# Performance work log

Hardware: AMD Instinct MI355X
Metric: run time of the kernel (lower is better)

Reference implementation:

```python
import math
import jax, jax.numpy as jnp
import numpy as np

B, S, T, C, H = 4, 100, 128, 256, 256
NH, DH = 4, 32            # num_attention_heads//2, hidden_size//num_attention_heads
AH = NH * DH              # all_head_size = 128
FH = 32                   # fire_hidden_size
MAX_SP, MAX_TM, MAX_DOY = 180.0, 365.0, 182.0


def _fire(dist, c, w1, w2, max_dist):
    # FIREDistanceBias: log-compressed distance -> MLP(1->FH, SiLU, FH->1, no bias)
    c = jnp.maximum(c, 0.0)
    d = jnp.log(c * dist + 1.0) / jnp.log(c * max_dist + 1.0)
    h = jax.nn.silu(d[..., None] * w1[:, 0])   # (..., FH)
    return h @ w2[0]                            # (...,)


def setup_inputs() -> dict:
    key = jax.random.key(0)
    ks = jax.random.split(key, 20)
    p = 0.02
    inp = {
        "hidden_states": jax.random.normal(ks[0], (B, S, T, H), jnp.float32),
        "source_embeddings": jax.random.normal(ks[1], (B, S, C, H), jnp.float32),
        "attention_mask": jnp.zeros((B, 1, 1, T, C), jnp.float32),
        "st_dist": jax.random.uniform(ks[2], (B, T, C, 2), jnp.float32)
                   * jnp.array([MAX_SP, MAX_TM], jnp.float32),
        "st_doy_dist": jax.random.uniform(ks[3], (B, T, C), jnp.float32) * MAX_DOY,
        # attention projections (Linear H->AH with bias), output dense (AH->H)
        "Wq": jax.random.normal(ks[4], (AH, H), jnp.float32) * p,
        "bq": jnp.zeros((AH,), jnp.float32),
        "Wk": jax.random.normal(ks[5], (AH, H), jnp.float32) * p,
        "bk": jnp.zeros((AH,), jnp.float32),
        "Wv": jax.random.normal(ks[6], (AH, H), jnp.float32) * p,
        "bv": jnp.zeros((AH,), jnp.float32),
        "Wo": jax.random.normal(ks[7], (H, AH), jnp.float32) * p,
        "bo": jnp.zeros((H,), jnp.float32),
        # FIRE params: spatial / temporal / seasonal
        "c_s": jnp.float32(100.0),
        "w1_s": jax.random.normal(ks[8], (FH, 1), jnp.float32) * 0.5,
        "w2_s": jax.random.normal(ks[9], (1, FH), jnp.float32) * 0.5,
        "c_t": jnp.float32(100.0),
        "w1_t": jax.random.normal(ks[10], (FH, 1), jnp.float32) * 0.5,
        "w2_t": jax.random.normal(ks[11], (1, FH), jnp.float32) * 0.5,
        "c_d": jnp.float32(100.0),
        "w1_d": jax.random.normal(ks[12], (FH, 1), jnp.float32) * 0.5,
        "w2_d": jax.random.normal(ks[13], (1, FH), jnp.float32) * 0.5,
        # per-species log scales (init zeros in torch)
        "s_log_scale": jnp.zeros((S,), jnp.float32),
        "t_log_scale": jnp.zeros((S,), jnp.float32),
    }
    return inp


def reference(hidden_states, source_embeddings, attention_mask, st_dist, st_doy_dist,
              Wq, bq, Wk, bk, Wv, bv, Wo, bo,
              c_s, w1_s, w2_s, c_t, w1_t, w2_t, c_d, w1_d, w2_d,
              s_log_scale, t_log_scale):
    # FIRE distance biases over (B, T, C)
    sb = _fire(st_dist[..., 0], c_s, w1_s, w2_s, MAX_SP)
    tb = _fire(st_dist[..., 1], c_t, w1_t, w2_t, MAX_TM)
    db = _fire(st_doy_dist, c_d, w1_d, w2_d, MAX_DOY)
    # (B, S, T, C): species-scaled spatial+temporal + seasonal bias
    bias = (sb[:, None] * jnp.exp(s_log_scale)[None, :, None, None]
            + tb[:, None] * jnp.exp(t_log_scale)[None, :, None, None]
            + db[:, None])

    # projections; split heads: (B,S,L,AH) -> (B,S,NH,L,DH)
    q = (hidden_states @ Wq.T + bq).reshape(B, S, T, NH, DH).transpose(0, 1, 3, 2, 4)
    k = (source_embeddings @ Wk.T + bk).reshape(B, S, C, NH, DH).transpose(0, 1, 3, 2, 4)
    v = (source_embeddings @ Wv.T + bv).reshape(B, S, C, NH, DH).transpose(0, 1, 3, 2, 4)

    scores = jnp.einsum('bshtd,bshcd->bshtc', q, k) / math.sqrt(DH)
    scores = scores + attention_mask + bias[:, :, None]   # mask (B,1,1,T,C), bias (B,S,1,T,C)
    probs = jax.nn.softmax(scores, axis=-1)
    ctx = jnp.einsum('bshtc,bshcd->bshtd', probs, v)
    ctx = ctx.transpose(0, 1, 3, 2, 4).reshape(B, S, T, AH)
    return ctx @ Wo.T + bo   # STCrossOutput dense (dropout=0, eval)
```

## Files before the change

### kernel.cpp

```cpp
#include <hip/hip_runtime.h>
#include <hip/hip_bf16.h>
#include <math.h>

#define Bdim 4
#define Sdim 100
#define Tdim 128
#define Cdim 256
#define Hdim 256
#define NHd  4
#define DHd  32
#define AHd  128

typedef short bf16x8 __attribute__((ext_vector_type(8)));
typedef float f32x4 __attribute__((ext_vector_type(4)));

#define WAITCNT_V(n) do { \
  asm volatile("s_waitcnt vmcnt(" #n ")" ::: "memory"); \
  __builtin_amdgcn_sched_barrier(0); \
} while (0)

__device__ __forceinline__ short f2b(float x) {
  unsigned u = __float_as_uint(x);
  unsigned r = (u + 0x7FFF + ((u >> 16) & 1)) >> 16;
  return (short)r;
}

__device__ __forceinline__ void split2(float x, short& hi, short& lo) {
  unsigned u = __float_as_uint(x) & 0xFFFF0000u;
  hi = (short)(u >> 16);
  lo = f2b(x - __uint_as_float(u));
}

__device__ __forceinline__ float fire_eval(float dist, float c,
                                           const float* __restrict__ w1,
                                           const float* __restrict__ w2,
                                           float maxd) {
  c = fmaxf(c, 0.0f);
  float d = logf(fmaf(c, dist, 1.0f)) / logf(fmaf(c, maxd, 1.0f));
  float acc = 0.0f;
#pragma unroll
  for (int j = 0; j < 32; ++j) {
    float x = d * w1[j];
    float h = x / (1.0f + expf(-x));
    acc = fmaf(h, w2[j], acc);
  }
  return acc;
}

__global__ __launch_bounds__(256) void fire_bias_kernel(
    const float* __restrict__ st_dist, const float* __restrict__ st_doy,
    const float* __restrict__ mask,
    const float* __restrict__ c_s, const float* __restrict__ w1_s, const float* __restrict__ w2_s,
    const float* __restrict__ c_t, const float* __restrict__ w1_t, const float* __restrict__ w2_t,
    const float* __restrict__ c_d, const float* __restrict__ w1_d, const float* __restrict__ w2_d,
    float4* __restrict__ pk) {
  int i = blockIdx.x * 256 + threadIdx.x;
  if (i >= Bdim * Tdim * Cdim) return;
  float2 dv = ((const float2*)st_dist)[i];
  float4 r;
  r.x = fire_eval(dv.x, c_s[0], w1_s, w2_s, 180.0f);
  r.y = fire_eval(dv.y, c_t[0], w1_t, w2_t, 365.0f);
  r.z = fire_eval(st_doy[i], c_d[0], w1_d, w2_d, 182.0f) + mask[i];
  r.w = 0.0f;
  pk[i] = r;
}

__global__ __launch_bounds__(256) void bias_combine(
    const float4* __restrict__ pk,
    const float* __restrict__ sls, const float* __restrict__ tls,
    float* __restrict__ bF) {
  const int l = threadIdx.x & 63;
  const int lr = l & 15, lg = l >> 4;
  const int nt = blockIdx.x * 4 + (threadIdx.x >> 6);
  const int wt = blockIdx.y;
  const int b  = blockIdx.z;
  const int c = nt * 16 + lr;
  float sb[4], tb[4], db[4];
#pragma unroll
  for (int r = 0; r < 4; ++r) {
    float4 v = pk[(size_t)b * Tdim * Cdim + (size_t)(wt * 16 + lg * 4 + r) * Cdim + c];
    sb[r] = v.x; tb[r] = v.y; db[r] = v.z;
  }
  for (int s = 0; s < Sdim; ++s) {
    float es = __expf(sls[s]), et = __expf(tls[s]);
    float4 o;
    o.x = fmaf(sb[0], es, fmaf(tb[0], et, db[0]));
    o.y = fmaf(sb[1], es, fmaf(tb[1], et, db[1]));
    o.z = fmaf(sb[2], es, fmaf(tb[2], et, db[2]));
    o.w = fmaf(sb[3], es, fmaf(tb[3], et, db[3]));
    size_t idx = ((((size_t)(b * Sdim + s) * 8 + wt) * 16 + nt) * 64 + l);
    *(float4*)(bF + idx * 4) = o;
  }
}

__global__ __launch_bounds__(256) void wsplit_pack(
    const float* __restrict__ Wq, const float* __restrict__ Wk,
    const float* __restrict__ Wv, const float* __restrict__ Wo,
    short* __restrict__ pack) {
  int which = blockIdx.y;
  const float* W = which == 0 ? Wq : which == 1 ? Wk : which == 2 ? Wv : Wo;
  int idx = blockIdx.x * 256 + threadIdx.x;
  int j = idx & 7;
  int l = (idx >> 3) & 63;
  int frag = idx >> 9;
  int nt, kk8, Kd;
  if (which == 3) { nt = frag & 15; kk8 = frag >> 4; Kd = 128; }
  else           { nt = frag & 7;  kk8 = frag >> 3; Kd = 256; }
  int n = nt * 16 + (l & 15);
  int k = kk8 * 32 + (l >> 4) * 8 + j;
  float val = W[(size_t)n * Kd + k];
  short h, lo_;
  if (which == 3) split2(val, h, lo_);
  else { h = f2b(val); lo_ = 0; }
  pack[(size_t)which * 65536 + idx] = h;
  pack[(size_t)which * 65536 + 32768 + idx] = lo_;
}


__global__ __launch_bounds__(256, 2) void proj_q_mfma(
    const float* __restrict__ A, const short* __restrict__ Wp,
    const float* __restrict__ bias, short* __restrict__ O, float scale) {
  __shared__ short wlds[2][8 * 512];
  const int tid = threadIdx.x;
  const int l = tid & 63, w = tid >> 6;
  const int lr = l & 15, lg = l >> 4;
  const int m0 = blockIdx.x * 128;
  const float* ap0 = A + (size_t)(m0 + w * 32 + lr) * 256 + lg * 8;
  const float* ap1 = ap0 + (size_t)16 * 256;

  auto stage = [&](int buf, int kk) {
#pragma unroll
    for (int r = 0; r < 2; ++r) {
      int f = w + 4 * r;
      const short* gsrc = Wp + ((size_t)(kk * 8 + f) * 64 + l) * 8;
      int loff = __builtin_amdgcn_readfirstlane(buf * 4096 + f * 512);
      __builtin_amdgcn_global_load_lds(gsrc, &wlds[0][0] + loff, 16, 0, 0);
    }
  };

  f32x4 acc[2][8] = {};
  stage(0, 0);
  float4 c0a = *(const float4*)ap0;
  float4 c0b = *(const float4*)(ap0 + 4);
  float4 c1a = *(const float4*)ap1;
  float4 c1b = *(const float4*)(ap1 + 4);
#pragma unroll
  for (int kk = 0; kk < 8; ++kk) {
    const int buf = kk & 1;
    float4 n0a, n0b, n1a, n1b;
    if (kk < 7) {
      stage(buf ^ 1, kk + 1);
      const int nk = (kk + 1) * 32;
      n0a = *(const float4*)(ap0 + nk);
      n0b = *(const float4*)(ap0 + nk + 4);
      n1a = *(const float4*)(ap1 + nk);
      n1b = *(const float4*)(ap1 + nk + 4);
    }
    bf16x8 af[2];
    {
      float a0[8] = {c0a.x, c0a.y, c0a.z, c0a.w, c0b.x, c0b.y, c0b.z, c0b.w};
      float a1[8] = {c1a.x, c1a.y, c1a.z, c1a.w, c1b.x, c1b.y, c1b.z, c1b.w};
#pragma unroll
      for (int e = 0; e < 8; ++e) { af[0][e] = f2b(a0[e]); af[1][e] = f2b(a1[e]); }
    }
    if (kk < 7) { WAITCNT_V(6); } else { WAITCNT_V(0); }
    __builtin_amdgcn_s_barrier();
    const short* lb = &wlds[0][0] + buf * 4096 + l * 8;
#pragma unroll
    for (int nt = 0; nt < 8; ++nt) {
      bf16x8 wv = *(const bf16x8*)(lb + nt * 512);
#pragma unroll
      for (int mi = 0; mi < 2; ++mi)
        acc[mi][nt] = __builtin_amdgcn_mfma_f32_16x16x32_bf16(af[mi], wv, acc[mi][nt], 0, 0, 0);
    }
    __builtin_amdgcn_s_barrier();
    if (kk < 7) { c0a = n0a; c0b = n0b; c1a = n1a; c1b = n1b; }
  }
#pragma unroll
  for (int mi = 0; mi < 2; ++mi)
#pragma unroll
    for (int nt = 0; nt < 8; ++nt)
#pragma unroll
      for (int r = 0; r < 4; ++r)
        O[(size_t)(m0 + w * 32 + mi * 16 + lg * 4 + r) * 128 + nt * 16 + lr] =
            f2b((acc[mi][nt][r] + bias[nt * 16 + lr]) * scale);
}

__global__ __launch_bounds__(256, 2) void proj_kv_mfma(
    const float* __restrict__ A,
    const short* __restrict__ Wkp, const float* __restrict__ bk,
    const short* __restrict__ Wvp, const float* __restrict__ bv,
    short* __restrict__ Ko, short* __restrict__ Vo) {
  __shared__ short wlds[2][16 * 512];
  const int tid = threadIdx.x;
  const int l = tid & 63, w = tid >> 6;
  const int lr = l & 15, lg = l >> 4;
  const int m0 = blockIdx.x * 128;
  const float* ap0 = A + (size_t)(m0 + w * 32 + lr) * 256 + lg * 8;
  const float* ap1 = ap0 + (size_t)16 * 256;

  auto stage = [&](int buf, int kk) {
#pragma unroll
    for (int r = 0; r < 4; ++r) {
      int f = w + 4 * r;
      const short* gsrc = ((f >> 3) ? Wvp : Wkp) + ((size_t)(kk * 8 + (f & 7)) * 64 + l) * 8;
      int loff = __builtin_amdgcn_readfirstlane(buf * 8192 + f * 512);
      __builtin_amdgcn_global_load_lds(gsrc, &wlds[0][0] + loff, 16, 0, 0);
    }
  };

  f32x4 accK[2][8] = {}, accV[2][8] = {};
  stage(0, 0);
  float4 c0a = *(const float4*)ap0;
  float4 c0b = *(const float4*)(ap0 + 4);
  float4 c1a = *(const float4*)ap1;
  float4 c1b = *(const float4*)(ap1 + 4);
#pragma unroll
  for (int kk = 0; kk < 8; ++kk) {
    const int buf = kk & 1;
    float4 n0a, n0b, n1a, n1b;
    if (kk < 7) {
      stage(buf ^ 1, kk + 1);
      const int nk = (kk + 1) * 32;
      n0a = *(const float4*)(ap0 + nk);
      n0b = *(const float4*)(ap0 + nk + 4);
      n1a = *(const float4*)(ap1 + nk);
      n1b = *(const float4*)(ap1 + nk + 4);
    }
    bf16x8 af[2];
    {
      float a0[8] = {c0a.x, c0a.y, c0a.z, c0a.w, c0b.x, c0b.y, c0b.z, c0b.w};
      float a1[8] = {c1a.x, c1a.y, c1a.z, c1a.w, c1b.x, c1b.y, c1b.z, c1b.w};
#pragma unroll
      for (int e = 0; e < 8; ++e) { af[0][e] = f2b(a0[e]); af[1][e] = f2b(a1[e]); }
    }
    if (kk < 7) { WAITCNT_V(8); } else { WAITCNT_V(0); }
    __builtin_amdgcn_s_barrier();
    const short* lb = &wlds[0][0] + buf * 8192 + l * 8;
#pragma unroll
    for (int nt = 0; nt < 8; ++nt) {
      bf16x8 kw = *(const bf16x8*)(lb + nt * 512);
      bf16x8 vw = *(const bf16x8*)(lb + (8 + nt) * 512);
#pragma unroll
      for (int mi = 0; mi < 2; ++mi) {
        accK[mi][nt] = __builtin_amdgcn_mfma_f32_16x16x32_bf16(af[mi], kw, accK[mi][nt], 0, 0, 0);
        accV[mi][nt] = __builtin_amdgcn_mfma_f32_16x16x32_bf16(af[mi], vw, accV[mi][nt], 0, 0, 0);
      }
    }
    __builtin_amdgcn_s_barrier();
    if (kk < 7) { c0a = n0a; c0b = n0b; c1a = n1a; c1b = n1b; }
  }
#pragma unroll
  for (int mi = 0; mi < 2; ++mi)
#pragma unroll
    for (int nt = 0; nt < 8; ++nt)
#pragma unroll
      for (int r = 0; r < 4; ++r) {
        size_t row = (size_t)(m0 + w * 32 + mi * 16 + lg * 4 + r) * 128 + nt * 16 + lr;
        Ko[row] = f2b(accK[mi][nt][r] + bk[nt * 16 + lr]);
        Vo[row] = f2b(accV[mi][nt][r] + bv[nt * 16 + lr]);
      }
}

__global__ __launch_bounds__(256, 2) void proj_o_mfma(
    const short* __restrict__ Ahi, const short* __restrict__ Alo,
    const short* __restrict__ Wp, const float* __restrict__ bias,
    float* __restrict__ O) {
  __shared__ short wlds[2][32 * 512];
  const int tid = threadIdx.x;
  const int l = tid & 63, w = tid >> 6;
  const int lr = l & 15, lg = l >> 4;
  const int m0 = blockIdx.x * 128;
  const short* ah0 = Ahi + (size_t)(m0 + w * 32 + lr) * 128 + lg * 8;
  const short* al0 = Alo + (size_t)(m0 + w * 32 + lr) * 128 + lg * 8;
  const short* ah1 = ah0 + (size_t)16 * 128;
  const short* al1 = al0 + (size_t)16 * 128;

  auto stage = [&](int buf, int kk) {
#pragma unroll
    for (int r = 0; r < 8; ++r) {
      int f = w + 4 * r;
      const short* gsrc = Wp + ((f >> 4) ? 32768 : 0)
                          + ((size_t)(kk * 16 + (f & 15)) * 64 + l) * 8;
      int loff = __builtin_amdgcn_readfirstlane(buf * 16384 + f * 512);
      __builtin_amdgcn_global_load_lds(gsrc, &wlds[0][0] + loff, 16, 0, 0);
    }
  };

  f32x4 acc[2][16] = {};
  stage(0, 0);
  bf16x8 ch0 = *(const bf16x8*)ah0;
  bf16x8 cl0 = *(const bf16x8*)al0;
  bf16x8 ch1 = *(const bf16x8*)ah1;
  bf16x8 cl1 = *(const bf16x8*)al1;
#pragma unroll
  for (int kk = 0; kk < 4; ++kk) {
    const int buf = kk & 1;
    bf16x8 nh0, nl0, nh1, nl1;
    if (kk < 3) {
      stage(buf ^ 1, kk + 1);
      const int nk = (kk + 1) * 32;
      nh0 = *(const bf16x8*)(ah0 + nk);
      nl0 = *(const bf16x8*)(al0 + nk);
      nh1 = *(const bf16x8*)(ah1 + nk);
      nl1 = *(const bf16x8*)(al1 + nk);
    }
    if (kk < 3) { WAITCNT_V(12); } else { WAITCNT_V(0); }
    __builtin_amdgcn_s_barrier();
    bf16x8 ahi[2] = {ch0, ch1};
    bf16x8 alo[2] = {cl0, cl1};
    const short* lb = &wlds[0][0] + buf * 16384 + l * 8;
#pragma unroll
    for (int nt = 0; nt < 16; ++nt) {
      bf16x8 whi = *(const bf16x8*)(lb + nt * 512);
      bf16x8 wlo = *(const bf16x8*)(lb + (16 + nt) * 512);
#pragma unroll
      for (int mi = 0; mi < 2; ++mi) {
        acc[mi][nt] = __builtin_amdgcn_mfma_f32_16x16x32_bf16(ahi[mi], whi, acc[mi][nt], 0, 0, 0);
        acc[mi][nt] = __builtin_amdgcn_mfma_f32_16x16x32_bf16(ahi[mi], wlo, acc[mi][nt], 0, 0, 0);
        acc[mi][nt] = __builtin_amdgcn_mfma_f32_16x16x32_bf16(alo[mi], whi, acc[mi][nt], 0, 0, 0);
      }
    }
    __builtin_amdgcn_s_barrier();
    if (kk < 3) { ch0 = nh0; cl0 = nl0; ch1 = nh1; cl1 = nl1; }
  }
#pragma unroll
  for (int mi = 0; mi < 2; ++mi)
#pragma unroll
    for (int nt = 0; nt < 16; ++nt)
#pragma unroll
      for (int r = 0; r < 4; ++r)
        O[(size_t)(m0 + w * 32 + mi * 16 + lg * 4 + r) * 256 + nt * 16 + lr] =
            acc[mi][nt][r] + bias[nt * 16 + lr];
}

__global__ __launch_bounds__(512, 2) void attn_mfma(
    const short* __restrict__ Qb, const short* __restrict__ Kb,
    const short* __restrict__ Vb,
    const float* __restrict__ bF,
    short* __restrict__ Chi, short* __restrict__ Clo) {
  __shared__ short vfrag[8][2][64][8];
  __shared__ short pbuf[8][16 * 36];

  const int tid = threadIdx.x;
  const int l = tid & 63;
  const int w = tid >> 6;
  const int lr = l & 15, lg = l >> 4;
  const int bid = blockIdx.x;
  const int xcd = bid & 7;
  const int i_  = bid >> 3;
  const int bs  = xcd * 50 + (i_ >> 2);
  const int h   = i_ & 3;

  const size_t kvbase = (size_t)bs * Cdim * AHd + h * DHd;
  const size_t qbase  = (size_t)bs * Tdim * AHd + h * DHd;

#pragma unroll
  for (int rep = 0; rep < 2; ++rep) {
    int chunk = tid * 2 + rep;
    int c = chunk >> 2, q = chunk & 3;
    bf16x8 v8 = *(const bf16x8*)(Vb + kvbase + (size_t)c * AHd + q * 8);
    int kc = c >> 5, nt = q >> 1;
    int lanebase = ((c & 31) >> 3) * 16 + (q & 1) * 8;
    int j = c & 7;
#pragma unroll
    for (int e = 0; e < 8; ++e) {
      int row = lanebase + e;
      int prow = row ^ ((row >> 4) << 1);
      vfrag[kc][nt][prow][j] = v8[e];
    }
  }
  __syncthreads();

  bf16x8 qf = *(const bf16x8*)(Qb + qbase + (size_t)(w * 16 + lr) * AHd + lg * 8);
  bf16x8 kf[16];
#pragma unroll
  for (int nt = 0; nt < 16; ++nt)
    kf[nt] = *(const bf16x8*)(Kb + kvbase + (size_t)(nt * 16 + lr) * AHd + lg * 8);

  const float4* bb = (const float4*)bF + ((size_t)bs * 8 + w) * 16 * 64 + l;
  f32x4 sacc[16];
#pragma unroll
  for (int nt = 0; nt < 16; ++nt) {
    float4 cv = bb[nt * 64];
    f32x4 cinit = {cv.x, cv.y, cv.z, cv.w};
    sacc[nt] = __builtin_amdgcn_mfma_f32_16x16x32_bf16(qf, kf[nt], cinit, 0, 0, 0);
  }

  float rinv[4];
#pragma unroll
  for (int nt = 0; nt < 16; ++nt)
#pragma unroll
    for (int r = 0; r < 4; ++r)
      sacc[nt][r] = __expf(sacc[nt][r]);
#pragma unroll
  for (int r = 0; r < 4; ++r) {
    float su = 0.f;
#pragma unroll
    for (int nt = 0; nt < 16; ++nt) su += sacc[nt][r];
#pragma unroll
    for (int off = 1; off < 16; off <<= 1) su += __shfl_xor(su, off);
    rinv[r] = 1.0f / su;
  }

  const f32x4 zero = {0.f, 0.f, 0.f, 0.f};
  f32x4 cacc[2] = {zero, zero};
  short* pb = &pbuf[w][0];
  const int lp = l ^ ((l >> 4) << 1);
#pragma unroll
  for (int kc = 0; kc < 8; ++kc) {
#pragma unroll
    for (int ntl = 0; ntl < 2; ++ntl) {
      int nt = kc * 2 + ntl;
#pragma unroll
      for (int r = 0; r < 4; ++r)
        pb[(lg * 4 + r) * 36 + ntl * 16 + lr] = f2b(sacc[nt][r]);
    }
    bf16x8 af = *(const bf16x8*)&pb[lr * 36 + lg * 8];
#pragma unroll
    for (int ntd = 0; ntd < 2; ++ntd) {
      bf16x8 vf = *(const bf16x8*)&vfrag[kc][ntd][lp][0];
      cacc[ntd] = __builtin_amdgcn_mfma_f32_16x16x32_bf16(af, vf, cacc[ntd], 0, 0, 0);
    }
  }

#pragma unroll
  for (int ntd = 0; ntd < 2; ++ntd)
#pragma unroll
    for (int r = 0; r < 4; ++r) {
      float val = cacc[ntd][r] * rinv[r];
      short h_, lo_;
      split2(val, h_, lo_);
      size_t idx = qbase + (size_t)(w * 16 + lg * 4 + r) * AHd + ntd * 16 + lr;
      Chi[idx] = h_;
      Clo[idx] = lo_;
    }
}

extern "C" void kernel_launch(void* const* d_in, const int* in_sizes, int n_in,
                              void* d_out, int out_size, void* d_ws, size_t ws_size,
                              hipStream_t stream) {
  const float* hs     = (const float*)d_in[0];
  const float* se     = (const float*)d_in[1];
  const float* mask   = (const float*)d_in[2];
  const float* stdist = (const float*)d_in[3];
  const float* stdoy  = (const float*)d_in[4];
  const float* Wq = (const float*)d_in[5];
  const float* bq = (const float*)d_in[6];
  const float* Wk = (const float*)d_in[7];
  const float* bk = (const float*)d_in[8];
  const float* Wv = (const float*)d_in[9];
  const float* bv = (const float*)d_in[10];
  const float* Wo = (const float*)d_in[11];
  const float* bo = (const float*)d_in[12];
  const float* c_s  = (const float*)d_in[13];
  const float* w1_s = (const float*)d_in[14];
  const float* w2_s = (const float*)d_in[15];
  const float* c_t  = (const float*)d_in[16];
  const float* w1_t = (const float*)d_in[17];
  const float* w2_t = (const float*)d_in[18];
  const float* c_d  = (const float*)d_in[19];
  const float* w1_d = (const float*)d_in[20];
  const float* w2_d = (const float*)d_in[21];
  const float* sls  = (const float*)d_in[22];
  const float* tls  = (const float*)d_in[23];
  float* out = (float*)d_out;

  float* ws = (float*)d_ws;
  const size_t BTC  = (size_t)Bdim * Tdim * Cdim;
  const size_t BSTC = (size_t)Bdim * Sdim * Tdim * Cdim;
  const size_t NQ   = (size_t)Bdim * Sdim * Tdim * AHd;
  const size_t NKV  = (size_t)Bdim * Sdim * Cdim * AHd;

  float4* pk  = (float4*)ws;
  float* bF   = ws + 4 * BTC;
  short* wpck = (short*)(bF + BSTC);
  short* Qb   = wpck + 262144;
  short* Kb   = Qb + NQ;
  short* Vb   = Kb + NKV;
  short* Chi  = Vb + NKV;
  short* Clo  = Chi + NQ;

  const int MQ  = Bdim * Sdim * Tdim;
  const int MKV = Bdim * Sdim * Cdim;

  fire_bias_kernel<<<(Bdim * Tdim * Cdim + 255) / 256, 256, 0, stream>>>(
      stdist, stdoy, mask, c_s, w1_s, w2_s, c_t, w1_t, w2_t, c_d, w1_d, w2_d, pk);

  bias_combine<<<dim3(4, 8, Bdim), 256, 0, stream>>>(pk, sls, tls, bF);

  wsplit_pack<<<dim3(128, 4), 256, 0, stream>>>(Wq, Wk, Wv, Wo, wpck);

  proj_q_mfma<<<dim3(MQ / 128), 256, 0, stream>>>(hs, wpck, bq, Qb,
                                                  0.17677669529663687f);
  proj_kv_mfma<<<dim3(MKV / 128), 256, 0, stream>>>(
      se, wpck + 65536, bk, wpck + 131072, bv, Kb, Vb);

  attn_mfma<<<dim3(Bdim * Sdim * NHd), 512, 0, stream>>>(
      Qb, Kb, Vb, bF, Chi, Clo);

  proj_o_mfma<<<dim3(MQ / 128), 256, 0, stream>>>(Chi, Clo, wpck + 196608, bo, out);
}
```

Measured before the change: 158.7 us.

## Merge Q, KV projections and bias combine into one launch; hoist Q/K loads

Combines the separate bias_combine, proj_q_mfma and proj_kv_mfma kernels into one kernel, phase1, whose blocks branch on block index to do KV projection, Q projection or bias expansion. This removes two launches and the tail gaps between them, so the short bias work can run alongside the GEMM blocks. In the attention kernel, the Q and K fragment global loads are moved ahead of the V staging into LDS so their latency overlaps it. In exchange the Q path now reserves the larger KV-sized LDS buffer, which may lower occupancy for those blocks, and the mixed block types can leave the load unevenly spread across CUs.

```diff
diff --git a/kernel.cpp b/kernel.cpp
--- a/kernel.cpp
+++ b/kernel.cpp
@@ -63,34 +63,6 @@
   r.z = fire_eval(st_doy[i], c_d[0], w1_d, w2_d, 182.0f) + mask[i];
   r.w = 0.0f;
   pk[i] = r;
-}
-
-__global__ __launch_bounds__(256) void bias_combine(
-    const float4* __restrict__ pk,
-    const float* __restrict__ sls, const float* __restrict__ tls,
-    float* __restrict__ bF) {
-  const int l = threadIdx.x & 63;
-  const int lr = l & 15, lg = l >> 4;
-  const int nt = blockIdx.x * 4 + (threadIdx.x >> 6);
-  const int wt = blockIdx.y;
-  const int b  = blockIdx.z;
-  const int c = nt * 16 + lr;
-  float sb[4], tb[4], db[4];
-#pragma unroll
-  for (int r = 0; r < 4; ++r) {
-    float4 v = pk[(size_t)b * Tdim * Cdim + (size_t)(wt * 16 + lg * 4 + r) * Cdim + c];
-    sb[r] = v.x; tb[r] = v.y; db[r] = v.z;
-  }
-  for (int s = 0; s < Sdim; ++s) {
-    float es = __expf(sls[s]), et = __expf(tls[s]);
-    float4 o;
-    o.x = fmaf(sb[0], es, fmaf(tb[0], et, db[0]));
-    o.y = fmaf(sb[1], es, fmaf(tb[1], et, db[1]));
-    o.z = fmaf(sb[2], es, fmaf(tb[2], et, db[2]));
-    o.w = fmaf(sb[3], es, fmaf(tb[3], et, db[3]));
-    size_t idx = ((((size_t)(b * Sdim + s) * 8 + wt) * 16 + nt) * 64 + l);
-    *(float4*)(bF + idx * 4) = o;
-  }
 }
 
 __global__ __launch_bounds__(256) void wsplit_pack(
@@ -116,150 +88,172 @@
   pack[(size_t)which * 65536 + 32768 + idx] = lo_;
 }
 
-
-__global__ __launch_bounds__(256, 2) void proj_q_mfma(
-    const float* __restrict__ A, const short* __restrict__ Wp,
-    const float* __restrict__ bias, short* __restrict__ O, float scale) {
-  __shared__ short wlds[2][8 * 512];
+__global__ __launch_bounds__(256, 2) void phase1(
+    const float* __restrict__ se,
+    const short* __restrict__ Wkp, const float* __restrict__ bk,
+    const short* __restrict__ Wvp, const float* __restrict__ bv,
+    short* __restrict__ Ko, short* __restrict__ Vo,
+    const float* __restrict__ hs, const short* __restrict__ Wqp,
+    const float* __restrict__ bq, short* __restrict__ Qb, float scale,
+    const float4* __restrict__ pk,
+    const float* __restrict__ sls, const float* __restrict__ tls,
+    float* __restrict__ bF) {
+  __shared__ short wlds[2][16 * 512];
+  const int bid = blockIdx.x;
   const int tid = threadIdx.x;
   const int l = tid & 63, w = tid >> 6;
   const int lr = l & 15, lg = l >> 4;
-  const int m0 = blockIdx.x * 128;
-  const float* ap0 = A + (size_t)(m0 + w * 32 + lr) * 256 + lg * 8;
-  const float* ap1 = ap0 + (size_t)16 * 256;
-
-  auto stage = [&](int buf, int kk) {
-#pragma unroll
-    for (int r = 0; r < 2; ++r) {
-      int f = w + 4 * r;
-      const short* gsrc = Wp + ((size_t)(kk * 8 + f) * 64 + l) * 8;
-      int loff = __builtin_amdgcn_readfirstlane(buf * 4096 + f * 512);
-      __builtin_amdgcn_global_load_lds(gsrc, &wlds[0][0] + loff, 16, 0, 0);
-    }
-  };
-
-  f32x4 acc[2][8] = {};
-  stage(0, 0);
-  float4 c0a = *(const float4*)ap0;
-  float4 c0b = *(const float4*)(ap0 + 4);
-  float4 c1a = *(const float4*)ap1;
-  float4 c1b = *(const float4*)(ap1 + 4);
-#pragma unroll
-  for (int kk = 0; kk < 8; ++kk) {
-    const int buf = kk & 1;
-    float4 n0a, n0b, n1a, n1b;
-    if (kk < 7) {
-      stage(buf ^ 1, kk + 1);
-      const int nk = (kk + 1) * 32;
-      n0a = *(const float4*)(ap0 + nk);
-      n0b = *(const float4*)(ap0 + nk + 4);
-      n1a = *(const float4*)(ap1 + nk);
-      n1b = *(const float4*)(ap1 + nk + 4);
-    }
-    bf16x8 af[2];
-    {
-      float a0[8] = {c0a.x, c0a.y, c0a.z, c0a.w, c0b.x, c0b.y, c0b.z, c0b.w};
-      float a1[8] = {c1a.x, c1a.y, c1a.z, c1a.w, c1b.x, c1b.y, c1b.z, c1b.w};
-#pragma unroll
-      for (int e = 0; e < 8; ++e) { af[0][e] = f2b(a0[e]); af[1][e] = f2b(a1[e]); }
-    }
-    if (kk < 7) { WAITCNT_V(6); } else { WAITCNT_V(0); }
-    __builtin_amdgcn_s_barrier();
-    const short* lb = &wlds[0][0] + buf * 4096 + l * 8;
-#pragma unroll
-    for (int nt = 0; nt < 8; ++nt) {
-      bf16x8 wv = *(const bf16x8*)(lb + nt * 512);
-#pragma unroll
-      for (int mi = 0; mi < 2; ++mi)
-        acc[mi][nt] = __builtin_amdgcn_mfma_f32_16x16x32_bf16(af[mi], wv, acc[mi][nt], 0, 0, 0);
-    }
-    __builtin_amdgcn_s_barrier();
-    if (kk < 7) { c0a = n0a; c0b = n0b; c1a = n1a; c1b = n1b; }
-  }
-#pragma unroll
-  for (int mi = 0; mi < 2; ++mi)
-#pragma unroll
-    for (int nt = 0; nt < 8; ++nt)
-#pragma unroll
-      for (int r = 0; r < 4; ++r)
-        O[(size_t)(m0 + w * 32 + mi * 16 + lg * 4 + r) * 128 + nt * 16 + lr] =
-            f2b((acc[mi][nt][r] + bias[nt * 16 + lr]) * scale);
-}
-
-__global__ __launch_bounds__(256, 2) void proj_kv_mfma(
-    const float* __restrict__ A,
-    const short* __restrict__ Wkp, const float* __restrict__ bk,
-    const short* __restrict__ Wvp, const float* __restrict__ bv,
-    short* __restrict__ Ko, short* __restrict__ Vo) {
-  __shared__ short wlds[2][16 * 512];
-  const int tid = threadIdx.x;
-  const int l = tid & 63, w = tid >> 6;
-  const int lr = l & 15, lg = l >> 4;
-  const int m0 = blockIdx.x * 128;
-  const float* ap0 = A + (size_t)(m0 + w * 32 + lr) * 256 + lg * 8;
-  const float* ap1 = ap0 + (size_t)16 * 256;
-
-  auto stage = [&](int buf, int kk) {
+
+  if (bid < 800) {
+    const int m0 = bid * 128;
+    const float* ap0 = se + (size_t)(m0 + w * 32 + lr) * 256 + lg * 8;
+    const float* ap1 = ap0 + (size_t)16 * 256;
+
+    auto stage = [&](int buf, int kk) {
+#pragma unroll
+      for (int r = 0; r < 4; ++r) {
+        int f = w + 4 * r;
+        const short* gsrc = ((f >> 3) ? Wvp : Wkp) + ((size_t)(kk * 8 + (f & 7)) * 64 + l) * 8;
+        int loff = __builtin_amdgcn_readfirstlane(buf * 8192 + f * 512);
+        __builtin_amdgcn_global_load_lds(gsrc, &wlds[0][0] + loff, 16, 0, 0);
+      }
+    };
+
+    f32x4 accK[2][8] = {}, accV[2][8] = {};
+    stage(0, 0);
+    float4 c0a = *(const float4*)ap0;
+    float4 c0b = *(const float4*)(ap0 + 4);
+    float4 c1a = *(const float4*)ap1;
+    float4 c1b = *(const float4*)(ap1 + 4);
+#pragma unroll
+    for (int kk = 0; kk < 8; ++kk) {
+      const int buf = kk & 1;
+      float4 n0a, n0b, n1a, n1b;
+      if (kk < 7) {
+        stage(buf ^ 1, kk + 1);
+        const int nk = (kk + 1) * 32;
+        n0a = *(const float4*)(ap0 + nk);
+        n0b = *(const float4*)(ap0 + nk + 4);
+        n1a = *(const float4*)(ap1 + nk);
+        n1b = *(const float4*)(ap1 + nk + 4);
+      }
+      bf16x8 af[2];
+      {
+        float a0[8] = {c0a.x, c0a.y, c0a.z, c0a.w, c0b.x, c0b.y, c0b.z, c0b.w};
+        float a1[8] = {c1a.x, c1a.y, c1a.z, c1a.w, c1b.x, c1b.y, c1b.z, c1b.w};
+#pragma unroll
+        for (int e = 0; e < 8; ++e) { af[0][e] = f2b(a0[e]); af[1][e] = f2b(a1[e]); }
+      }
+      if (kk < 7) { WAITCNT_V(8); } else { WAITCNT_V(0); }
+      __builtin_amdgcn_s_barrier();
+      const short* lb = &wlds[0][0] + buf * 8192 + l * 8;
+#pragma unroll
+      for (int nt = 0; nt < 8; ++nt) {
+        bf16x8 kw = *(const bf16x8*)(lb + nt * 512);
+        bf16x8 vw = *(const bf16x8*)(lb + (8 + nt) * 512);
+#pragma unroll
+        for (int mi = 0; mi < 2; ++mi) {
+          accK[mi][nt] = __builtin_amdgcn_mfma_f32_16x16x32_bf16(af[mi], kw, accK[mi][nt], 0, 0, 0);
+          accV[mi][nt] = __builtin_amdgcn_mfma_f32_16x16x32_bf16(af[mi], vw, accV[mi][nt], 0, 0, 0);
+        }
+      }
+      __builtin_amdgcn_s_barrier();
+      if (kk < 7) { c0a = n0a; c0b = n0b; c1a = n1a; c1b = n1b; }
+    }
+#pragma unroll
+    for (int mi = 0; mi < 2; ++mi)
+#pragma unroll
+      for (int nt = 0; nt < 8; ++nt)
+#pragma unroll
+        for (int r = 0; r < 4; ++r) {
+          size_t row = (size_t)(m0 + w * 32 + mi * 16 + lg * 4 + r) * 128 + nt * 16 + lr;
+          Ko[row] = f2b(accK[mi][nt][r] + bk[nt * 16 + lr]);
+          Vo[row] = f2b(accV[mi][nt][r] + bv[nt * 16 + lr]);
+        }
+  } else if (bid < 1200) {
+    const int m0 = (bid - 800) * 128;
+    const float* ap0 = hs + (size_t)(m0 + w * 32 + lr) * 256 + lg * 8;
+    const float* ap1 = ap0 + (size_t)16 * 256;
+
+    auto stage = [&](int buf, int kk) {
+#pragma unroll
+      for (int r = 0; r < 2; ++r) {
+        int f = w + 4 * r;
+        const short* gsrc = Wqp + ((size_t)(kk * 8 + f) * 64 + l) * 8;
+        int loff = __builtin_amdgcn_readfirstlane(buf * 8192 + f * 512);
+        __builtin_amdgcn_global_load_lds(gsrc, &wlds[0][0] + loff, 16, 0, 0);
+      }
+    };
+
+    f32x4 acc[2][8] = {};
+    stage(0, 0);
+    float4 c0a = *(const float4*)ap0;
+    float4 c0b = *(const float4*)(ap0 + 4);
+    float4 c1a = *(const float4*)ap1;
+    float4 c1b = *(const float4*)(ap1 + 4);
+#pragma unroll
+    for (int kk = 0; kk < 8; ++kk) {
+      const int buf = kk & 1;
+      float4 n0a, n0b, n1a, n1b;
+      if (kk < 7) {
+        stage(buf ^ 1, kk + 1);
+        const int nk = (kk + 1) * 32;
+        n0a = *(const float4*)(ap0 + nk);
+        n0b = *(const float4*)(ap0 + nk + 4);
+        n1a = *(const float4*)(ap1 + nk);
+        n1b = *(const float4*)(ap1 + nk + 4);
+      }
+      bf16x8 af[2];
+      {
+        float a0[8] = {c0a.x, c0a.y, c0a.z, c0a.w, c0b.x, c0b.y, c0b.z, c0b.w};
+        float a1[8] = {c1a.x, c1a.y, c1a.z, c1a.w, c1b.x, c1b.y, c1b.z, c1b.w};
+#pragma unroll
+        for (int e = 0; e < 8; ++e) { af[0][e] = f2b(a0[e]); af[1][e] = f2b(a1[e]); }
+      }
+      if (kk < 7) { WAITCNT_V(6); } else { WAITCNT_V(0); }
+      __builtin_amdgcn_s_barrier();
+      const short* lb = &wlds[0][0] + buf * 8192 + l * 8;
+#pragma unroll
+      for (int nt = 0; nt < 8; ++nt) {
+        bf16x8 wv = *(const bf16x8*)(lb + nt * 512);
+#pragma unroll
+        for (int mi = 0; mi < 2; ++mi)
+          acc[mi][nt] = __builtin_amdgcn_mfma_f32_16x16x32_bf16(af[mi], wv, acc[mi][nt], 0, 0, 0);
+      }
+      __builtin_amdgcn_s_barrier();
+      if (kk < 7) { c0a = n0a; c0b = n0b; c1a = n1a; c1b = n1b; }
+    }
+#pragma unroll
+    for (int mi = 0; mi < 2; ++mi)
+#pragma unroll
+      for (int nt = 0; nt < 8; ++nt)
+#pragma unroll
+        for (int r = 0; r < 4; ++r)
+          Qb[(size_t)(m0 + w * 32 + mi * 16 + lg * 4 + r) * 128 + nt * 16 + lr] =
+              f2b((acc[mi][nt][r] + bq[nt * 16 + lr]) * scale);
+  } else {
+    const int bb_ = bid - 1200;
+    const int nt = (bb_ & 3) * 4 + w;
+    const int wt = (bb_ >> 2) & 7;
+    const int b  = bb_ >> 5;
+    const int c = nt * 16 + lr;
+    float sb[4], tb[4], db[4];
 #pragma unroll
     for (int r = 0; r < 4; ++r) {
-      int f = w + 4 * r;
-      const short* gsrc = ((f >> 3) ? Wvp : Wkp) + ((size_t)(kk * 8 + (f & 7)) * 64 + l) * 8;
-      int loff = __builtin_amdgcn_readfirstlane(buf * 8192 + f * 512);
-      __builtin_amdgcn_global_load_lds(gsrc, &wlds[0][0] + loff, 16, 0, 0);
-    }
-  };
-
-  f32x4 accK[2][8] = {}, accV[2][8] = {};
-  stage(0, 0);
-  float4 c0a = *(const float4*)ap0;
-  float4 c0b = *(const float4*)(ap0 + 4);
-  float4 c1a = *(const float4*)ap1;
-  float4 c1b = *(const float4*)(ap1 + 4);
-#pragma unroll
-  for (int kk = 0; kk < 8; ++kk) {
-    const int buf = kk & 1;
-    float4 n0a, n0b, n1a, n1b;
-    if (kk < 7) {
-      stage(buf ^ 1, kk + 1);
-      const int nk = (kk + 1) * 32;
-      n0a = *(const float4*)(ap0 + nk);
-      n0b = *(const float4*)(ap0 + nk + 4);
-      n1a = *(const float4*)(ap1 + nk);
-      n1b = *(const float4*)(ap1 + nk + 4);
-    }
-    bf16x8 af[2];
-    {
-      float a0[8] = {c0a.x, c0a.y, c0a.z, c0a.w, c0b.x, c0b.y, c0b.z, c0b.w};
-      float a1[8] = {c1a.x, c1a.y, c1a.z, c1a.w, c1b.x, c1b.y, c1b.z, c1b.w};
-#pragma unroll
-      for (int e = 0; e < 8; ++e) { af[0][e] = f2b(a0[e]); af[1][e] = f2b(a1[e]); }
-    }
-    if (kk < 7) { WAITCNT_V(8); } else { WAITCNT_V(0); }
-    __builtin_amdgcn_s_barrier();
-    const short* lb = &wlds[0][0] + buf * 8192 + l * 8;
-#pragma unroll
-    for (int nt = 0; nt < 8; ++nt) {
-      bf16x8 kw = *(const bf16x8*)(lb + nt * 512);
-      bf16x8 vw = *(const bf16x8*)(lb + (8 + nt) * 512);
-#pragma unroll
-      for (int mi = 0; mi < 2; ++mi) {
-        accK[mi][nt] = __builtin_amdgcn_mfma_f32_16x16x32_bf16(af[mi], kw, accK[mi][nt], 0, 0, 0);
-        accV[mi][nt] = __builtin_amdgcn_mfma_f32_16x16x32_bf16(af[mi], vw, accV[mi][nt], 0, 0, 0);
-      }
-    }
-    __builtin_amdgcn_s_barrier();
-    if (kk < 7) { c0a = n0a; c0b = n0b; c1a = n1a; c1b = n1b; }
-  }
-#pragma unroll
-  for (int mi = 0; mi < 2; ++mi)
-#pragma unroll
-    for (int nt = 0; nt < 8; ++nt)
-#pragma unroll
-      for (int r = 0; r < 4; ++r) {
-        size_t row = (size_t)(m0 + w * 32 + mi * 16 + lg * 4 + r) * 128 + nt * 16 + lr;
-        Ko[row] = f2b(accK[mi][nt][r] + bk[nt * 16 + lr]);
-        Vo[row] = f2b(accV[mi][nt][r] + bv[nt * 16 + lr]);
-      }
+      float4 v = pk[(size_t)b * Tdim * Cdim + (size_t)(wt * 16 + lg * 4 + r) * Cdim + c];
+      sb[r] = v.x; tb[r] = v.y; db[r] = v.z;
+    }
+    for (int s = 0; s < Sdim; ++s) {
+      float es = __expf(sls[s]), et = __expf(tls[s]);
+      float4 o;
+      o.x = fmaf(sb[0], es, fmaf(tb[0], et, db[0]));
+      o.y = fmaf(sb[1], es, fmaf(tb[1], et, db[1]));
+      o.z = fmaf(sb[2], es, fmaf(tb[2], et, db[2]));
+      o.w = fmaf(sb[3], es, fmaf(tb[3], et, db[3]));
+      size_t idx = ((((size_t)(b * Sdim + s) * 8 + wt) * 16 + nt) * 64 + l);
+      *(float4*)(bF + idx * 4) = o;
+    }
+  }
 }
 
 __global__ __launch_bounds__(256, 2) void proj_o_mfma(
@@ -355,6 +349,12 @@
   const size_t kvbase = (size_t)bs * Cdim * AHd + h * DHd;
   const size_t qbase  = (size_t)bs * Tdim * AHd + h * DHd;
 
+  bf16x8 qf = *(const bf16x8*)(Qb + qbase + (size_t)(w * 16 + lr) * AHd + lg * 8);
+  bf16x8 kf[16];
+#pragma unroll
+  for (int nt = 0; nt < 16; ++nt)
+    kf[nt] = *(const bf16x8*)(Kb + kvbase + (size_t)(nt * 16 + lr) * AHd + lg * 8);
+
 #pragma unroll
   for (int rep = 0; rep < 2; ++rep) {
     int chunk = tid * 2 + rep;
@@ -371,12 +371,6 @@
     }
   }
   __syncthreads();
-
-  bf16x8 qf = *(const bf16x8*)(Qb + qbase + (size_t)(w * 16 + lr) * AHd + lg * 8);
-  bf16x8 kf[16];
-#pragma unroll
-  for (int nt = 0; nt < 16; ++nt)
-    kf[nt] = *(const bf16x8*)(Kb + kvbase + (size_t)(nt * 16 + lr) * AHd + lg * 8);
 
   const float4* bb = (const float4*)bF + ((size_t)bs * 8 + w) * 16 * 64 + l;
   f32x4 sacc[16];
@@ -482,19 +476,16 @@
   short* Clo  = Chi + NQ;
 
   const int MQ  = Bdim * Sdim * Tdim;
-  const int MKV = Bdim * Sdim * Cdim;
 
   fire_bias_kernel<<<(Bdim * Tdim * Cdim + 255) / 256, 256, 0, stream>>>(
       stdist, stdoy, mask, c_s, w1_s, w2_s, c_t, w1_t, w2_t, c_d, w1_d, w2_d, pk);
 
-  bias_combine<<<dim3(4, 8, Bdim), 256, 0, stream>>>(pk, sls, tls, bF);
-
   wsplit_pack<<<dim3(128, 4), 256, 0, stream>>>(Wq, Wk, Wv, Wo, wpck);
 
-  proj_q_mfma<<<dim3(MQ / 128), 256, 0, stream>>>(hs, wpck, bq, Qb,
-                                                  0.17677669529663687f);
-  proj_kv_mfma<<<dim3(MKV / 128), 256, 0, stream>>>(
-      se, wpck + 65536, bk, wpck + 131072, bv, Kb, Vb);
+  phase1<<<dim3(1328), 256, 0, stream>>>(
+      se, wpck + 65536, bk, wpck + 131072, bv, Kb, Vb,
+      hs, wpck, bq, Qb, 0.17677669529663687f,
+      pk, sls, tls, bF);
 
   attn_mfma<<<dim3(Bdim * Sdim * NHd), 512, 0, stream>>>(
       Qb, Kb, Vb, bF, Chi, Clo);
```

Result: no change. 156.0 us (-1.7%).
